# Performance work log

Measured on AMD Instinct MI355X. Metric: run time of the kernel, lower is better.

The kernel has to match this reference:

```python
import jax, jax.numpy as jnp
import numpy as np

N_EMBD = 2048
NUM_GROUPS = 8
EXPERTS_PER_GROUP = 8
ROUTER_TEMPERATURE = 1.0
N_TOKENS = 16384


def setup_inputs() -> dict:
    key = jax.random.key(0)
    kx, kg, ke = jax.random.split(key, 3)
    x = jax.random.normal(kx, (N_TOKENS, N_EMBD), dtype=jnp.float32)
    # nn.Linear(in, out, bias=False) stores weight as [out, in]; kaiming-uniform-ish scale
    bound = 1.0 / np.sqrt(N_EMBD)
    group_gate_w = jax.random.uniform(kg, (NUM_GROUPS, N_EMBD), dtype=jnp.float32,
                                      minval=-bound, maxval=bound)
    expert_gate_w = jax.random.uniform(ke, (NUM_GROUPS * EXPERTS_PER_GROUP, N_EMBD),
                                       dtype=jnp.float32, minval=-bound, maxval=bound)
    return {"x": x, "group_gate_w": group_gate_w, "expert_gate_w": expert_gate_w}


def reference(x, group_gate_w, expert_gate_w):
    N = x.shape[0]
    G = NUM_GROUPS
    E_g = EXPERTS_PER_GROUP
    inv_temp = 1.0 / ROUTER_TEMPERATURE

    # Level 1: group routing
    group_logits = jnp.einsum('nd,gd->ng', x, group_gate_w)            # [N, G]
    group_probs = jax.nn.softmax(group_logits * inv_temp, axis=-1)     # [N, G]
    group_mask = group_probs >= (1.0 / G)                              # [N, G]

    # Level 2: expert routing within each group
    expert_logits = jnp.einsum('nd,ed->ne', x, expert_gate_w)          # [N, G*E_g]
    expert_logits = expert_logits.reshape(N, G, E_g)
    expert_probs = jax.nn.softmax(expert_logits * inv_temp, axis=-1)   # [N, G, E_g]
    expert_mask = expert_probs >= (1.0 / E_g)                          # [N, G, E_g]

    valid_mask_3d = group_mask[:, :, None] & expert_mask               # [N, G, E_g]
    selected_weights_3d = (group_probs[:, :, None] * expert_probs) * valid_mask_3d.astype(x.dtype)

    valid_mask = valid_mask_3d.reshape(N, G * E_g)
    selected_weights = selected_weights_3d.reshape(N, G * E_g)
    weight_sum = jnp.clip(jnp.sum(selected_weights, axis=-1, keepdims=True), 1e-9, None)
    normalized_weights = selected_weights / weight_sum
    return (valid_mask, normalized_weights)
```

## Files before the change

kernel.cpp:

```cpp
#include <hip/hip_runtime.h>


#define NT 16384
#define NE 2048
#define NTH 256
#define NBLK 1024
#define WS_HALFS 163840

typedef _Float16 v8h __attribute__((ext_vector_type(8)));
typedef float    v4f __attribute__((ext_vector_type(4)));

__global__ __launch_bounds__(256, 1)
void prep(const float* __restrict__ gw, const float* __restrict__ ew,
          _Float16* __restrict__ wf)
{
    const int f = blockIdx.x * 256 + threadIdx.x;
    const int j  = f & 7;
    const int sl = (f >> 3) & 63;
    const int ks = (f >> 9) & 63;
    const int g  = f >> 15;
    const int q  = sl >> 4, m = sl & 15;
    const int gate = g * 16 + m;
    const int k = ks * 32 + q * 8 + j;
    float v = 0.f;
    if (gate < 64)      v = ew[gate * NE + k];
    else if (gate < 72) v = gw[(gate - 64) * NE + k];
    const _Float16 h = (_Float16)v;
    wf[f]            = h;
    wf[WS_HALFS + f] = (_Float16)((v - (float)h) * 2048.0f);
}

__global__ __launch_bounds__(NTH, 4)
void router(const float* __restrict__ x, const _Float16* __restrict__ wf,
            float* __restrict__ out)
{
    __shared__ __align__(16) char sm[20736];
    const int tid  = threadIdx.x;
    const int lane = tid & 63;
    const int w    = tid >> 6;
    const int t0   = blockIdx.x * 16;

    const float* xp = x + (size_t)(t0 + (lane & 15)) * NE + (lane >> 4) * 8;

    v4f accH[5], accC[5];
    #pragma unroll
    for (int g = 0; g < 5; ++g) { accH[g] = (v4f)(0.f); accC[g] = (v4f)(0.f); }

    float4 xr0, xr1;
    auto xload = [&](int s) {
        const float* p = xp + (size_t)(w * 16 + s) * 32;
        xr0 = *(const float4*)(p);
        xr1 = *(const float4*)(p + 4);
    };

    xload(0);
    for (int s = 0; s < 16; ++s) {
        v8h Bh, Bl;
        {
            const float xv[8] = {xr0.x, xr0.y, xr0.z, xr0.w, xr1.x, xr1.y, xr1.z, xr1.w};
            #pragma unroll
            for (int j = 0; j < 8; ++j) {
                const _Float16 hh = (_Float16)xv[j];
                Bh[j] = hh;
                Bl[j] = (_Float16)((xv[j] - (float)hh) * 2048.0f);
            }
        }
        if (s + 1 < 16) xload(s + 1);

        const int ks = w * 16 + s;
        const _Float16* base = wf + ((size_t)ks * 64 + lane) * 8;
        #pragma unroll
        for (int g = 0; g < 5; ++g) {
            const v8h Ah = *(const v8h*)(base + g * 32768);
            const v8h Al = *(const v8h*)(base + g * 32768 + WS_HALFS);
            accH[g] = __builtin_amdgcn_mfma_f32_16x16x32_f16(Ah, Bh, accH[g], 0, 0, 0);
            accC[g] = __builtin_amdgcn_mfma_f32_16x16x32_f16(Ah, Bl, accC[g], 0, 0, 0);
            accC[g] = __builtin_amdgcn_mfma_f32_16x16x32_f16(Al, Bh, accC[g], 0, 0, 0);
        }
    }

    float part[5][4];
    #pragma unroll
    for (int g = 0; g < 5; ++g)
        #pragma unroll
        for (int r = 0; r < 4; ++r)
            part[g][r] = accH[g][r] + accC[g][r] * (1.0f / 2048.0f);

    float* red = (float*)sm;
    if (w > 0) {
        #pragma unroll
        for (int g = 0; g < 5; ++g)
            #pragma unroll
            for (int r = 0; r < 4; ++r)
                red[(((w - 1) * 5 + g) * 4 + r) * 64 + lane] = part[g][r];
    }
    __syncthreads();
    float* la = (float*)(sm + 15360);
    if (w == 0) {
        #pragma unroll
        for (int g = 0; g < 5; ++g)
            #pragma unroll
            for (int r = 0; r < 4; ++r) {
                float v = part[g][r]
                        + red[((0 * 5 + g) * 4 + r) * 64 + lane]
                        + red[((1 * 5 + g) * 4 + r) * 64 + lane]
                        + red[((2 * 5 + g) * 4 + r) * 64 + lane];
                const int gate  = g * 16 + (lane >> 4) * 4 + r;
                const int token = lane & 15;
                la[token * 84 + gate] = v;
            }
    }
    __syncthreads();

    if (lane < 4) {
        const int token = w * 4 + lane;
        const float* lg = la + token * 84;
        float* M  = (float*)sm + token * 64;
        float* Wn = (float*)(sm + 4096) + token * 64;

        float gpb[8];
        float gmax = lg[64];
        #pragma unroll
        for (int g = 1; g < 8; ++g) gmax = fmaxf(gmax, lg[64 + g]);
        float gsum = 0.f;
        #pragma unroll
        for (int g = 0; g < 8; ++g) { gpb[g] = __expf(lg[64 + g] - gmax); gsum += gpb[g]; }
        const float ginv = 1.f / gsum;

        float sel[64];
        float wsum = 0.f;
        #pragma unroll
        for (int g = 0; g < 8; ++g) {
            const float gp_ = gpb[g] * ginv;
            float emax = lg[g * 8];
            #pragma unroll
            for (int j = 1; j < 8; ++j) emax = fmaxf(emax, lg[g * 8 + j]);
            float ep[8]; float esum = 0.f;
            #pragma unroll
            for (int j = 0; j < 8; ++j) { ep[j] = __expf(lg[g * 8 + j] - emax); esum += ep[j]; }
            const float einv = 1.f / esum;
            const bool gm = gp_ >= 0.125f;
            #pragma unroll
            for (int j = 0; j < 8; ++j) {
                const float pe = ep[j] * einv;
                const bool v = gm && (pe >= 0.125f);
                const float ww = v ? gp_ * pe : 0.f;
                M[g * 8 + j] = v ? 1.f : 0.f;
                sel[g * 8 + j] = ww;
                wsum += ww;
            }
        }
        const float inv = 1.f / fmaxf(wsum, 1e-9f);
        #pragma unroll
        for (int e = 0; e < 64; ++e) Wn[e] = sel[e] * inv;
    }
    __syncthreads();

    const float4* M4 = (const float4*)sm;
    const float4* W4 = (const float4*)(sm + 4096);
    float4* o0 = (float4*)(out + (size_t)t0 * 64);
    float4* o1 = (float4*)(out + (size_t)NT * 64 + (size_t)t0 * 64);
    o0[tid] = M4[tid];
    o1[tid] = W4[tid];
}

extern "C" void kernel_launch(void* const* d_in, const int* in_sizes, int n_in,
                              void* d_out, int out_size, void* d_ws, size_t ws_size,
                              hipStream_t stream) {
    const float* x  = (const float*)d_in[0];
    const float* gw = (const float*)d_in[1];
    const float* ew = (const float*)d_in[2];
    float* out = (float*)d_out;
    _Float16* wf = (_Float16*)d_ws;
    (void)ws_size; (void)in_sizes; (void)n_in; (void)out_size;

    prep<<<dim3(640), dim3(256), 0, stream>>>(gw, ew, wf);
    router<<<dim3(NBLK), dim3(NTH), 0, stream>>>(x, wf, out);
}
```

Before: 225.7 us.

## Stage weights and split-fp16 x tiles through double-buffered LDS with 64-token blocks

Each block now covers 64 tokens with 512 threads. Weight chunks (interleaved hi/lo fp16 from a re-laid-out prep) and x chunks (converted to hi/lo fp16 once) are staged through double-buffered shared memory, with a swizzled layout so every wave reads its MFMA operands from LDS. Before, each wave fetched weights straight from global memory for only 16 tokens. The aim is to reuse the weights across four times more tokens and cut redundant global and L2 traffic. The cost is 75KB of LDS per block, which limits occupancy, plus a barrier per chunk, and only 256 blocks cover the GPU.

Result: slower. 271.2 us (+20.2%).

```diff
diff --git a/kernel.cpp b/kernel.cpp
--- a/kernel.cpp
+++ b/kernel.cpp
@@ -3,9 +3,13 @@
 
 #define NT 16384
 #define NE 2048
-#define NTH 256
-#define NBLK 1024
-#define WS_HALFS 163840
+#define NTH 512
+#define NBLK 256
+#define NCHUNK 32
+#define WCH 20480
+#define XCH 16384
+#define XOFF 40960
+#define LDS_BYTES 76800
 
 typedef _Float16 v8h __attribute__((ext_vector_type(8)));
 typedef float    v4f __attribute__((ext_vector_type(4)));
@@ -14,70 +18,108 @@
 void prep(const float* __restrict__ gw, const float* __restrict__ ew,
           _Float16* __restrict__ wf)
 {
-    const int f = blockIdx.x * 256 + threadIdx.x;
-    const int j  = f & 7;
-    const int sl = (f >> 3) & 63;
-    const int ks = (f >> 9) & 63;
-    const int g  = f >> 15;
-    const int q  = sl >> 4, m = sl & 15;
+    const int t = blockIdx.x * 256 + threadIdx.x;
+    const int j    = t & 7;
+    const int sl   = (t >> 3) & 63;
+    const int rest = t >> 9;
+    const int g    = rest % 5;
+    const int ks   = rest / 5;
+    const int m = sl & 15, q = sl >> 4;
     const int gate = g * 16 + m;
     const int k = ks * 32 + q * 8 + j;
     float v = 0.f;
     if (gate < 64)      v = ew[gate * NE + k];
     else if (gate < 72) v = gw[(gate - 64) * NE + k];
     const _Float16 h = (_Float16)v;
-    wf[f]            = h;
-    wf[WS_HALFS + f] = (_Float16)((v - (float)h) * 2048.0f);
+    const int o = (((ks * 5 + g) * 2) * 64 + sl) * 8 + j;
+    wf[o]       = h;
+    wf[o + 512] = (_Float16)((v - (float)h) * 2048.0f);
 }
 
 __global__ __launch_bounds__(NTH, 4)
 void router(const float* __restrict__ x, const _Float16* __restrict__ wf,
             float* __restrict__ out)
 {
-    __shared__ __align__(16) char sm[20736];
+    __shared__ __align__(16) char sm[LDS_BYTES];
     const int tid  = threadIdx.x;
     const int lane = tid & 63;
     const int w    = tid >> 6;
-    const int t0   = blockIdx.x * 16;
-
-    const float* xp = x + (size_t)(t0 + (lane & 15)) * NE + (lane >> 4) * 8;
+    const int tt   = w >> 1, s2 = w & 1;
+    const int t0   = blockIdx.x * 64;
+
+    const int xtok = tid >> 3, xks = tid & 7;
+    const float* xsrc = x + (size_t)(t0 + xtok) * NE + xks * 8;
+    const int xa16 = (((xtok >> 4) * 2 + (xks >> 2)) * 2) * 64
+                   + (((xks & 3) * 16 + (xtok & 15)) ^ xks);
+
+    uint4  wr[3];
+    float4 xr[2][2];
+
+    auto wload = [&](int c) {
+        const char* src = (const char*)wf + (size_t)c * WCH;
+        wr[0] = *(const uint4*)(src + (0 * 512 + tid) * 16);
+        wr[1] = *(const uint4*)(src + (1 * 512 + tid) * 16);
+        if (tid < 256) wr[2] = *(const uint4*)(src + (1024 + tid) * 16);
+    };
+    auto wcommit = [&](int buf) {
+        char* dst = sm + buf * WCH;
+        *(uint4*)(dst + (0 * 512 + tid) * 16) = wr[0];
+        *(uint4*)(dst + (1 * 512 + tid) * 16) = wr[1];
+        if (tid < 256) *(uint4*)(dst + (1024 + tid) * 16) = wr[2];
+    };
+    auto xload = [&](int c) {
+        const float* p = xsrc + c * 64;
+        xr[c & 1][0] = *(const float4*)(p);
+        xr[c & 1][1] = *(const float4*)(p + 4);
+    };
+    auto xcommit = [&](int c, int buf) {
+        const float4 a = xr[c & 1][0], b = xr[c & 1][1];
+        const float v[8] = {a.x, a.y, a.z, a.w, b.x, b.y, b.z, b.w};
+        v8h h, l;
+        #pragma unroll
+        for (int j = 0; j < 8; ++j) {
+            const _Float16 hh = (_Float16)v[j];
+            h[j] = hh;
+            l[j] = (_Float16)((v[j] - (float)hh) * 2048.0f);
+        }
+        char* xb = sm + XOFF + buf * XCH;
+        *(v8h*)(xb + xa16 * 16)        = h;
+        *(v8h*)(xb + (xa16 + 64) * 16) = l;
+    };
 
     v4f accH[5], accC[5];
     #pragma unroll
     for (int g = 0; g < 5; ++g) { accH[g] = (v4f)(0.f); accC[g] = (v4f)(0.f); }
 
-    float4 xr0, xr1;
-    auto xload = [&](int s) {
-        const float* p = xp + (size_t)(w * 16 + s) * 32;
-        xr0 = *(const float4*)(p);
-        xr1 = *(const float4*)(p + 4);
-    };
-
-    xload(0);
-    for (int s = 0; s < 16; ++s) {
-        v8h Bh, Bl;
+    const int xrd = (((tt * 2 + s2) * 2) * 64 + (lane ^ (s2 * 4 + (lane >> 4)))) * 16;
+    const int wrd = ((s2 * 5) * 2) * 1024 + lane * 16;
+
+    wload(0); xload(0);
+    wcommit(0); xcommit(0, 0);
+    xload(1);
+
+    for (int c = 0; c < NCHUNK; ++c) {
+        __syncthreads();
+        if (c + 1 < NCHUNK) wload(c + 1);
+        if (c + 2 < NCHUNK) xload(c + 2);
         {
-            const float xv[8] = {xr0.x, xr0.y, xr0.z, xr0.w, xr1.x, xr1.y, xr1.z, xr1.w};
-            #pragma unroll
-            for (int j = 0; j < 8; ++j) {
-                const _Float16 hh = (_Float16)xv[j];
-                Bh[j] = hh;
-                Bl[j] = (_Float16)((xv[j] - (float)hh) * 2048.0f);
+            const char* xb = sm + XOFF + (c & 1) * XCH;
+            const char* wb = sm + (c & 1) * WCH;
+            const v8h Bh = *(const v8h*)(xb + xrd);
+            const v8h Bl = *(const v8h*)(xb + xrd + 1024);
+            #pragma unroll
+            for (int g = 0; g < 5; ++g) {
+                const char* wpg = wb + wrd + g * 2048;
+                const v8h Ah = *(const v8h*)(wpg);
+                const v8h Al = *(const v8h*)(wpg + 1024);
+                accH[g] = __builtin_amdgcn_mfma_f32_16x16x32_f16(Ah, Bh, accH[g], 0, 0, 0);
+                accC[g] = __builtin_amdgcn_mfma_f32_16x16x32_f16(Ah, Bl, accC[g], 0, 0, 0);
+                accC[g] = __builtin_amdgcn_mfma_f32_16x16x32_f16(Al, Bh, accC[g], 0, 0, 0);
             }
         }
-        if (s + 1 < 16) xload(s + 1);
-
-        const int ks = w * 16 + s;
-        const _Float16* base = wf + ((size_t)ks * 64 + lane) * 8;
-        #pragma unroll
-        for (int g = 0; g < 5; ++g) {
-            const v8h Ah = *(const v8h*)(base + g * 32768);
-            const v8h Al = *(const v8h*)(base + g * 32768 + WS_HALFS);
-            accH[g] = __builtin_amdgcn_mfma_f32_16x16x32_f16(Ah, Bh, accH[g], 0, 0, 0);
-            accC[g] = __builtin_amdgcn_mfma_f32_16x16x32_f16(Ah, Bl, accC[g], 0, 0, 0);
-            accC[g] = __builtin_amdgcn_mfma_f32_16x16x32_f16(Al, Bh, accC[g], 0, 0, 0);
-        }
-    }
+        if (c + 1 < NCHUNK) { wcommit((c + 1) & 1); xcommit(c + 1, (c + 1) & 1); }
+    }
+    __syncthreads();
 
     float part[5][4];
     #pragma unroll
@@ -87,36 +129,33 @@
             part[g][r] = accH[g][r] + accC[g][r] * (1.0f / 2048.0f);
 
     float* red = (float*)sm;
-    if (w > 0) {
+    if (s2 == 1) {
         #pragma unroll
         for (int g = 0; g < 5; ++g)
             #pragma unroll
             for (int r = 0; r < 4; ++r)
-                red[(((w - 1) * 5 + g) * 4 + r) * 64 + lane] = part[g][r];
-    }
-    __syncthreads();
-    float* la = (float*)(sm + 15360);
-    if (w == 0) {
+                red[((tt * 5 + g) * 4 + r) * 64 + lane] = part[g][r];
+    }
+    __syncthreads();
+    float* la = (float*)(sm + 20480);
+    if (s2 == 0) {
         #pragma unroll
         for (int g = 0; g < 5; ++g)
             #pragma unroll
             for (int r = 0; r < 4; ++r) {
-                float v = part[g][r]
-                        + red[((0 * 5 + g) * 4 + r) * 64 + lane]
-                        + red[((1 * 5 + g) * 4 + r) * 64 + lane]
-                        + red[((2 * 5 + g) * 4 + r) * 64 + lane];
+                const float v = part[g][r] + red[((tt * 5 + g) * 4 + r) * 64 + lane];
                 const int gate  = g * 16 + (lane >> 4) * 4 + r;
-                const int token = lane & 15;
+                const int token = tt * 16 + (lane & 15);
                 la[token * 84 + gate] = v;
             }
     }
     __syncthreads();
 
-    if (lane < 4) {
-        const int token = w * 4 + lane;
+    if (lane < 8) {
+        const int token = w * 8 + lane;
         const float* lg = la + token * 84;
-        float* M  = (float*)sm + token * 64;
-        float* Wn = (float*)(sm + 4096) + token * 64;
+        float* M  = (float*)(sm + 41984) + token * 64;
+        float* Wn = (float*)(sm + 58368) + token * 64;
 
         float gpb[8];
         float gmax = lg[64];
@@ -156,12 +195,14 @@
     }
     __syncthreads();
 
-    const float4* M4 = (const float4*)sm;
-    const float4* W4 = (const float4*)(sm + 4096);
+    const float4* M4 = (const float4*)(sm + 41984);
+    const float4* W4 = (const float4*)(sm + 58368);
     float4* o0 = (float4*)(out + (size_t)t0 * 64);
     float4* o1 = (float4*)(out + (size_t)NT * 64 + (size_t)t0 * 64);
-    o0[tid] = M4[tid];
-    o1[tid] = W4[tid];
+    o0[tid]       = M4[tid];
+    o0[tid + 512] = M4[tid + 512];
+    o1[tid]       = W4[tid];
+    o1[tid + 512] = W4[tid + 512];
 }
 
 extern "C" void kernel_launch(void* const* d_in, const int* in_sizes, int n_in,
```
